# Kernel tuning notes

Measured on AMD Instinct MI355X. Metric: run time of the kernel, lower is better.

The kernel has to match this reference:

```python
import jax, jax.numpy as jnp
import numpy as np
import math

C = 91                      # num classes incl. background
BBOX_CLIP = math.log(1000.0 / 16.0)
IMG_H, IMG_W = 800.0, 800.0
SCORE_THRESH = 0.05
NMS_THRESH = 0.5
DETS_PER_IMG = 100
MIN_SIZE = 0.01
WX, WY, WW, WH = 10.0, 10.0, 5.0, 5.0   # bbox_reg_weights


def setup_inputs() -> dict:
    key = jax.random.key(0)
    ks = jax.random.split(key, 8)
    B, N, F_IN, HID = 4, 2048, 12544, 1024
    box_features = jax.random.normal(ks[0], (B, N, F_IN), jnp.float32) * 0.1
    # valid proposal boxes inside an 800x800 image: x1y1 in [0,600], wh in [10,200]
    xy = jax.random.uniform(ks[1], (B, N, 2), jnp.float32, minval=0.0, maxval=600.0)
    wh = jax.random.uniform(ks[2], (B, N, 2), jnp.float32, minval=10.0, maxval=200.0)
    proposals = jnp.concatenate([xy, xy + wh], axis=-1)
    def sc(k, sh, fan):
        return jax.random.normal(k, sh, jnp.float32) * (1.0 / np.sqrt(fan))
    return {
        'box_features': box_features,
        'proposals': proposals,
        'fc6_w': sc(ks[3], (F_IN, HID), F_IN), 'fc6_b': jnp.zeros((HID,), jnp.float32),
        'fc7_w': sc(ks[4], (HID, HID), HID),   'fc7_b': jnp.zeros((HID,), jnp.float32),
        'cls_w': sc(ks[5], (HID, C), HID),     'cls_b': jnp.zeros((C,), jnp.float32),
        'bbox_w': sc(ks[6], (HID, 4 * C), HID), 'bbox_b': jnp.zeros((4 * C,), jnp.float32),
    }


def decode_boxes(rel, props):
    w = props[:, 2] - props[:, 0]
    h = props[:, 3] - props[:, 1]
    cx = props[:, 0] + 0.5 * w
    cy = props[:, 1] + 0.5 * h
    dx = rel[..., 0] / WX
    dy = rel[..., 1] / WY
    dw = jnp.minimum(rel[..., 2] / WW, BBOX_CLIP)
    dh = jnp.minimum(rel[..., 3] / WH, BBOX_CLIP)
    pcx = dx * w[:, None] + cx[:, None]
    pcy = dy * h[:, None] + cy[:, None]
    pw = jnp.exp(dw) * w[:, None]
    ph = jnp.exp(dh) * h[:, None]
    return jnp.stack([pcx - 0.5 * pw, pcy - 0.5 * ph,
                      pcx + 0.5 * pw, pcy + 0.5 * ph], axis=-1)


def postprocess_one(logits, regr, props):
    # logits [N,C], regr [N,4C], props [N,4] -> padded top-DETS_PER_IMG detections
    N = logits.shape[0]
    boxes = decode_boxes(regr.reshape(N, C, 4), props)        # [N,C,4]
    scores = jax.nn.softmax(logits, axis=-1)                  # [N,C]
    # clip_boxes_to_image
    x = jnp.clip(boxes[..., 0::2], 0.0, IMG_W)
    y = jnp.clip(boxes[..., 1::2], 0.0, IMG_H)
    boxes = jnp.stack([x[..., 0], y[..., 0], x[..., 1], y[..., 1]], axis=-1)
    # drop background class, flatten candidates
    boxes = boxes[:, 1:].reshape(-1, 4)                       # [M,4], M=N*(C-1)
    scores = scores[:, 1:].reshape(-1)                        # [M]
    labels = jnp.broadcast_to(jnp.arange(1, C, dtype=jnp.int32)[None, :],
                              (N, C - 1)).reshape(-1)         # [M]
    # score threshold + remove_small_boxes (invalidate instead of dynamic gather)
    bw = boxes[:, 2] - boxes[:, 0]
    bh = boxes[:, 3] - boxes[:, 1]
    valid = (scores > SCORE_THRESH) & (bw >= MIN_SIZE) & (bh >= MIN_SIZE)
    s0 = jnp.where(valid, scores, -jnp.inf)
    # batched_nms via per-class coordinate offset
    offset = labels.astype(boxes.dtype)[:, None] * (max(IMG_H, IMG_W) + 1.0)
    ob = boxes + offset
    area = (ob[:, 2] - ob[:, 0]) * (ob[:, 3] - ob[:, 1])

    def body(sc_cur, _):
        best = jnp.argmax(sc_cur)
        bb = ob[best]
        lt = jnp.maximum(ob[:, :2], bb[:2])
        rb = jnp.minimum(ob[:, 2:], bb[2:])
        inter = jnp.prod(jnp.maximum(rb - lt, 0.0), axis=-1)
        union = jnp.maximum(area + area[best] - inter, 1e-6)
        iou = inter / union
        sc_new = jnp.where(iou > NMS_THRESH, -jnp.inf, sc_cur)
        return sc_new, (best, sc_cur[best])

    _, (keep, kept_s) = jax.lax.scan(body, s0, None, length=DETS_PER_IMG)
    ok = jnp.isfinite(kept_s)
    out_boxes = jnp.where(ok[:, None], boxes[keep], 0.0)      # [D,4]
    out_scores = jnp.where(ok, kept_s, 0.0)                   # [D]
    out_labels = jnp.where(ok, labels[keep], 0)               # [D] int32
    return out_boxes, out_scores, out_labels


def reference(box_features, proposals, fc6_w, fc6_b, fc7_w, fc7_b,
              cls_w, cls_b, bbox_w, bbox_b):
    # TwoMLPHead
    h = jax.nn.relu(box_features @ fc6_w + fc6_b)             # [B,N,1024]
    h = jax.nn.relu(h @ fc7_w + fc7_b)
    # FastRCNNPredictor
    logits = h @ cls_w + cls_b                                # [B,N,C]
    regr = h @ bbox_w + bbox_b                                # [B,N,4C]
    boxes, scores, labels = jax.vmap(postprocess_one)(logits, regr, proposals)
    return boxes, scores, labels
```

## Files before the change

### kernel.cpp

```cpp
#include <hip/hip_runtime.h>
#include <math.h>

#define NIMG   4
#define NPROP  2048
#define MTOT   8192
#define FIN    12544
#define HID    1024
#define NC     91
#define NCB    512
#define DETS   100
#define CAPMAX (NPROP * (NC - 1))
#define VLDS   2560

typedef __attribute__((ext_vector_type(8))) short short8;
typedef __attribute__((ext_vector_type(4))) float f32x4;

__device__ __forceinline__ unsigned short f2bf(float f) {
  union { float f; unsigned u; } v; v.f = f;
  unsigned r = v.u + 0x7fffu + ((v.u >> 16) & 1u);
  return (unsigned short)(r >> 16);
}

__device__ __forceinline__ unsigned cvtpk(float lo, float hi) {
  unsigned r;
  asm("v_cvt_pk_bf16_f32 %0, %1, %2" : "=v"(r) : "v"(lo), "v"(hi));
  return r;
}

__device__ __forceinline__ void gload_lds16(const void* g, void* l) {
  __builtin_amdgcn_global_load_lds((__attribute__((address_space(1))) void*)(g),
                                   (__attribute__((address_space(3))) void*)(l), 16, 0, 0);
}

__global__ void transpose_cvt(const float* __restrict__ in, unsigned short* __restrict__ out,
                              int K, int N, int row_off, int out_ld) {
  __shared__ float tile[32][33];
  int k0 = blockIdx.y * 32, n0 = blockIdx.x * 32;
  int tx = threadIdx.x, ty = threadIdx.y;
#pragma unroll
  for (int i = 0; i < 4; ++i) {
    int r = ty + i * 8;
    if (k0 + r < K && n0 + tx < N)
      tile[r][tx] = in[(size_t)(k0 + r) * N + (n0 + tx)];
  }
  __syncthreads();
#pragma unroll
  for (int i = 0; i < 4; ++i) {
    int r = ty + i * 8;
    if (n0 + r < N && k0 + tx < K)
      out[(size_t)(row_off + n0 + r) * out_ld + (k0 + tx)] = f2bf(tile[tx][r]);
  }
}

__global__ void prep_misc(unsigned short* __restrict__ Wcbt, float* __restrict__ bias_cb,
                          const float* __restrict__ cls_b, const float* __restrict__ bbox_b,
                          int* __restrict__ ccount) {
  int i = blockIdx.x * blockDim.x + threadIdx.x;
  int stride = gridDim.x * blockDim.x;
  for (int j = i; j < 57 * 1024; j += stride) Wcbt[455 * 1024 + j] = 0;
  for (int j = i; j < NCB; j += stride)
    bias_cb[j] = (j < 91) ? cls_b[j] : ((j < 455) ? bbox_b[j - 91] : 0.0f);
  if (i < NIMG) ccount[i] = 0;
}

template <bool AFP32, bool RELU, bool OUTBF16>
__global__ __launch_bounds__(256) void gemm_nt(const void* __restrict__ Av,
                                               const unsigned short* __restrict__ Bt,
                                               const float* __restrict__ bias,
                                               void* __restrict__ Cv,
                                               int M, int N, int K) {
  __shared__ __align__(16) unsigned short As[128 * 64];
  __shared__ __align__(16) unsigned short Bs[128 * 64];
  const int tid  = threadIdx.x;
  const int lane = tid & 63;
  const int wid  = tid >> 6;
  const int wm   = (wid >> 1) * 64;
  const int wn   = (wid & 1) * 64;
  const int m0   = blockIdx.y * 128, n0 = blockIdx.x * 128;
  const int lcol = lane & 15;
  const int lk8  = (lane >> 4) * 8;

  f32x4 acc[4][4];
#pragma unroll
  for (int a = 0; a < 4; ++a)
#pragma unroll
    for (int b = 0; b < 4; ++b)
#pragma unroll
      for (int r = 0; r < 4; ++r) acc[a][b][r] = 0.0f;

  const int st_r  = lane >> 3;
  const int st_kc = (lane & 7) << 3;

  for (int k0 = 0; k0 < K; k0 += 64) {
#pragma unroll
    for (int i = 0; i < 4; ++i) {
      int chunk = (wid << 2) | i;
      int r = (chunk << 3) | st_r;
      gload_lds16(Bt + (size_t)(n0 + r) * K + k0 + st_kc, Bs + (chunk << 9));
    }
    if constexpr (AFP32) {
#pragma unroll
      for (int i = 0; i < 4; ++i) {
        int s   = tid + (i << 8);
        int row = s >> 3;
        int kc  = (s & 7) << 3;
        const float* gp = (const float*)Av + (size_t)(m0 + row) * K + (k0 + kc);
        float4 u = *(const float4*)gp;
        float4 w = *(const float4*)(gp + 4);
        union { unsigned u32[4]; short8 s8; } pk;
        pk.u32[0] = cvtpk(u.x, u.y);
        pk.u32[1] = cvtpk(u.z, u.w);
        pk.u32[2] = cvtpk(w.x, w.y);
        pk.u32[3] = cvtpk(w.z, w.w);
        *(short8*)&As[row * 64 + kc] = pk.s8;
      }
    } else {
#pragma unroll
      for (int i = 0; i < 4; ++i) {
        int chunk = (wid << 2) | i;
        int r = (chunk << 3) | st_r;
        gload_lds16((const unsigned short*)Av + (size_t)(m0 + r) * K + k0 + st_kc,
                    As + (chunk << 9));
      }
    }
    __syncthreads();
#pragma unroll
    for (int kk = 0; kk < 64; kk += 32) {
      short8 af[4], bf[4];
#pragma unroll
      for (int im = 0; im < 4; ++im)
        af[im] = *(const short8*)&As[(wm + im * 16 + lcol) * 64 + kk + lk8];
#pragma unroll
      for (int in = 0; in < 4; ++in)
        bf[in] = *(const short8*)&Bs[(wn + in * 16 + lcol) * 64 + kk + lk8];
#pragma unroll
      for (int im = 0; im < 4; ++im)
#pragma unroll
        for (int in = 0; in < 4; ++in)
          acc[im][in] = __builtin_amdgcn_mfma_f32_16x16x32_bf16(af[im], bf[in], acc[im][in], 0, 0, 0);
    }
    __syncthreads();
  }

  const int r0 = (lane >> 4) * 4;
#pragma unroll
  for (int im = 0; im < 4; ++im) {
#pragma unroll
    for (int in = 0; in < 4; ++in) {
      int gn = n0 + wn + in * 16 + lcol;
      float bv = bias[gn];
#pragma unroll
      for (int r = 0; r < 4; ++r) {
        int gm = m0 + wm + im * 16 + r0 + r;
        float vv = acc[im][in][r] + bv;
        if (RELU) vv = fmaxf(vv, 0.0f);
        if (OUTBF16) ((unsigned short*)Cv)[(size_t)gm * N + gn] = f2bf(vv);
        else         ((float*)Cv)[(size_t)gm * N + gn] = vv;
      }
    }
  }
}

__global__ void candgen(const float* __restrict__ out3, const float* __restrict__ props,
                        float* __restrict__ cscore, float* __restrict__ cbox,
                        int* __restrict__ clabel, int* __restrict__ ccount, int CAP) {
  int gw   = (blockIdx.x * blockDim.x + threadIdx.x) >> 6;
  int lane = threadIdx.x & 63;
  if (gw >= MTOT) return;
  int img = gw >> 11;
  const float* row = out3 + (size_t)gw * NCB;

  float l0 = row[lane];
  float l1 = (lane < NC - 64) ? row[64 + lane] : -INFINITY;
  float mx = fmaxf(l0, l1);
#pragma unroll
  for (int off = 32; off; off >>= 1) mx = fmaxf(mx, __shfl_xor(mx, off));
  float e0 = expf(l0 - mx);
  float e1 = (lane < NC - 64) ? expf(l1 - mx) : 0.0f;
  float den = e0 + e1;
#pragma unroll
  for (int off = 32; off; off >>= 1) den += __shfl_xor(den, off);
  float inv = 1.0f / den;

  float4 p = *(const float4*)(props + (size_t)gw * 4);
  float w = p.z - p.x, h = p.w - p.y;
  float cx = p.x + 0.5f * w, cy = p.y + 0.5f * h;

#pragma unroll
  for (int half = 0; half < 2; ++half) {
    int c = (half << 6) + lane;
    float s = (half ? e1 : e0) * inv;
    if (c >= 1 && c < NC && s > 0.05f) {
      float dx = row[91 + c * 4 + 0] * 0.1f;
      float dy = row[91 + c * 4 + 1] * 0.1f;
      float dw = fminf(row[91 + c * 4 + 2] * 0.2f, 4.135166556742356f);
      float dh = fminf(row[91 + c * 4 + 3] * 0.2f, 4.135166556742356f);
      float pcx = dx * w + cx, pcy = dy * h + cy;
      float pw = expf(dw) * w, ph = expf(dh) * h;
      float x1 = fminf(fmaxf(pcx - 0.5f * pw, 0.0f), 800.0f);
      float x2 = fminf(fmaxf(pcx + 0.5f * pw, 0.0f), 800.0f);
      float y1 = fminf(fmaxf(pcy - 0.5f * ph, 0.0f), 800.0f);
      float y2 = fminf(fmaxf(pcy + 0.5f * ph, 0.0f), 800.0f);
      if (x2 - x1 >= 0.01f && y2 - y1 >= 0.01f) {
        int idx = atomicAdd(&ccount[img], 1);
        if (idx < CAP) {
          size_t o = (size_t)img * CAP + idx;
          cscore[o] = s;
          clabel[o] = c;
          cbox[o * 4 + 0] = x1; cbox[o * 4 + 1] = y1;
          cbox[o * 4 + 2] = x2; cbox[o * 4 + 3] = y2;
        }
      }
    }
  }
}

__global__ __launch_bounds__(256) void nms_kernel(float* __restrict__ cscore, const float* __restrict__ cbox,
                           const int* __restrict__ clabel, const int* __restrict__ ccount,
                           float* __restrict__ out, int CAP) {
  int img = blockIdx.x;
  int tid = threadIdx.x;
  int lane = tid & 63, wid = tid >> 6;
  int V = ccount[img]; if (V > CAP) V = CAP;
  int VL = V < VLDS ? V : VLDS;
  float* sc = cscore + (size_t)img * CAP;
  const float* bx = cbox + (size_t)img * CAP * 4;
  const int* lb = clabel + (size_t)img * CAP;
  float* ob  = out + (size_t)img * DETS * 4;
  float* osd = out + (size_t)NIMG * DETS * 4 + (size_t)img * DETS;
  float* ol  = out + (size_t)NIMG * DETS * 5 + (size_t)img * DETS;

  for (int t = tid; t < DETS; t += blockDim.x) {
    ob[t * 4 + 0] = 0.0f; ob[t * 4 + 1] = 0.0f; ob[t * 4 + 2] = 0.0f; ob[t * 4 + 3] = 0.0f;
    osd[t] = 0.0f; ol[t] = 0.0f;
  }

  __shared__ float sx1[VLDS], sy1[VLDS], sx2[VLDS], sy2[VLDS], sar[VLDS], ssc[VLDS];
  __shared__ float rs[4]; __shared__ int ri[4];
  __shared__ float bbs[6];
  __shared__ int   bbest;

  for (int t = tid; t < VL; t += blockDim.x) {
    float4 b = *(const float4*)&bx[(size_t)t * 4];
    float offv = (float)lb[t] * 801.0f;
    sx1[t] = b.x + offv; sy1[t] = b.y + offv;
    sx2[t] = b.z + offv; sy2[t] = b.w + offv;
    sar[t] = (b.z - b.x) * (b.w - b.y);
    ssc[t] = sc[t];
  }
  __syncthreads();

  for (int d = 0; d < DETS; ++d) {
    float bs = -INFINITY; int bi = -1;
    for (int t = tid; t < VL; t += blockDim.x) { float v = ssc[t]; if (v > bs) { bs = v; bi = t; } }
    if (V > VLDS)
      for (int t = VLDS + tid; t < V; t += blockDim.x) { float v = sc[t]; if (v > bs) { bs = v; bi = t; } }
#pragma unroll
    for (int off = 32; off; off >>= 1) {
      float osf = __shfl_xor(bs, off); int oi = __shfl_xor(bi, off);
      if (osf > bs) { bs = osf; bi = oi; }
    }
    if (lane == 0) { rs[wid] = bs; ri[wid] = bi; }
    __syncthreads();
    if (tid == 0) {
      float b0 = rs[0]; int i0 = ri[0];
      for (int wv = 1; wv < 4; ++wv) if (rs[wv] > b0) { b0 = rs[wv]; i0 = ri[wv]; }
      if (i0 < 0 || !(b0 > -INFINITY)) {
        bbest = -1;
      } else {
        bbest = i0;
        float ox1, oy1, ox2, oy2, ar;
        if (i0 < VLDS) { ox1 = sx1[i0]; oy1 = sy1[i0]; ox2 = sx2[i0]; oy2 = sy2[i0]; ar = sar[i0]; }
        else {
          float4 b = *(const float4*)&bx[(size_t)i0 * 4];
          float offv = (float)lb[i0] * 801.0f;
          ox1 = b.x + offv; oy1 = b.y + offv; ox2 = b.z + offv; oy2 = b.w + offv;
          ar = (b.z - b.x) * (b.w - b.y);
        }
        bbs[0] = ox1; bbs[1] = oy1; bbs[2] = ox2; bbs[3] = oy2; bbs[4] = ar;
        float4 rb = *(const float4*)&bx[(size_t)i0 * 4];
        ob[d * 4 + 0] = rb.x; ob[d * 4 + 1] = rb.y; ob[d * 4 + 2] = rb.z; ob[d * 4 + 3] = rb.w;
        osd[d] = b0;
        ol[d] = (float)lb[i0];
      }
    }
    __syncthreads();
    if (bbest < 0) break;
    float bx1 = bbs[0], by1 = bbs[1], bx2 = bbs[2], by2 = bbs[3], barea = bbs[4];
    for (int t = tid; t < VL; t += blockDim.x) {
      float ltx = fmaxf(sx1[t], bx1), lty = fmaxf(sy1[t], by1);
      float rbx = fminf(sx2[t], bx2), rby = fminf(sy2[t], by2);
      float inter = fmaxf(rbx - ltx, 0.0f) * fmaxf(rby - lty, 0.0f);
      float uni = fmaxf(sar[t] + barea - inter, 1e-6f);
      if (inter / uni > 0.5f) ssc[t] = -INFINITY;
    }
    if (V > VLDS) {
      for (int t = VLDS + tid; t < V; t += blockDim.x) {
        float4 b = *(const float4*)&bx[(size_t)t * 4];
        float offv = (float)lb[t] * 801.0f;
        float tx1 = b.x + offv, ty1 = b.y + offv, tx2 = b.z + offv, ty2 = b.w + offv;
        float ltx = fmaxf(tx1, bx1), lty = fmaxf(ty1, by1);
        float rbx = fminf(tx2, bx2), rby = fminf(ty2, by2);
        float inter = fmaxf(rbx - ltx, 0.0f) * fmaxf(rby - lty, 0.0f);
        float areat = (tx2 - tx1) * (ty2 - ty1);
        float uni = fmaxf(areat + barea - inter, 1e-6f);
        if (inter / uni > 0.5f) sc[t] = -INFINITY;
      }
    }
    __syncthreads();
  }
}

extern "C" void kernel_launch(void* const* d_in, const int* in_sizes, int n_in,
                              void* d_out, int out_size, void* d_ws, size_t ws_size,
                              hipStream_t stream) {
  const float* box_features = (const float*)d_in[0];
  const float* proposals    = (const float*)d_in[1];
  const float* fc6_w = (const float*)d_in[2];
  const float* fc6_b = (const float*)d_in[3];
  const float* fc7_w = (const float*)d_in[4];
  const float* fc7_b = (const float*)d_in[5];
  const float* cls_w = (const float*)d_in[6];
  const float* cls_b = (const float*)d_in[7];
  const float* bbox_w = (const float*)d_in[8];
  const float* bbox_b = (const float*)d_in[9];

  char* ws = (char*)d_ws;
  size_t off = 0;
  unsigned short* W6t  = (unsigned short*)(ws + off); off += (size_t)HID * FIN * 2;
  unsigned short* W7t  = (unsigned short*)(ws + off); off += (size_t)HID * HID * 2;
  unsigned short* Wcbt = (unsigned short*)(ws + off); off += (size_t)NCB * HID * 2;
  float* bias_cb       = (float*)(ws + off);          off += (size_t)NCB * 4;
  int*   ccount        = (int*)(ws + off);            off += 256;
  unsigned short* h1   = (unsigned short*)(ws + off); off += (size_t)MTOT * HID * 2;
  unsigned short* h2   = (unsigned short*)(ws + off); off += (size_t)MTOT * HID * 2;
  float* out3          = (float*)(ws + off);          off += (size_t)MTOT * NCB * 4;

  int CAP = CAPMAX;
  if (ws_size > off) {
    size_t avail = ws_size - off;
    size_t cap_ws = avail / 96;
    if (cap_ws < (size_t)CAP) CAP = (int)cap_ws;
  } else {
    CAP = 0;
  }
  float* cscore = (float*)(ws + off);
  int*   clabel = (int*)(ws + off + (size_t)NIMG * CAP * 4);
  float* cbox   = (float*)(ws + off + (size_t)NIMG * CAP * 8);

  transpose_cvt<<<dim3(HID / 32, FIN / 32), dim3(32, 8), 0, stream>>>(fc6_w, W6t, FIN, HID, 0, FIN);
  transpose_cvt<<<dim3(HID / 32, HID / 32), dim3(32, 8), 0, stream>>>(fc7_w, W7t, HID, HID, 0, HID);
  transpose_cvt<<<dim3(3,  HID / 32), dim3(32, 8), 0, stream>>>(cls_w,  Wcbt, HID, 91,  0,  HID);
  transpose_cvt<<<dim3(12, HID / 32), dim3(32, 8), 0, stream>>>(bbox_w, Wcbt, HID, 364, 91, HID);
  prep_misc<<<64, 256, 0, stream>>>(Wcbt, bias_cb, cls_b, bbox_b, ccount);

  gemm_nt<true,  true,  true ><<<dim3(HID / 128, MTOT / 128), 256, 0, stream>>>(
      box_features, W6t, fc6_b, h1, MTOT, HID, FIN);
  gemm_nt<false, true,  true ><<<dim3(HID / 128, MTOT / 128), 256, 0, stream>>>(
      h1, W7t, fc7_b, h2, MTOT, HID, HID);
  gemm_nt<false, false, false><<<dim3(NCB / 128, MTOT / 128), 256, 0, stream>>>(
      h2, Wcbt, bias_cb, out3, MTOT, NCB, HID);

  candgen<<<(MTOT * 64) / 256, 256, 0, stream>>>(out3, proposals, cscore, cbox, clabel, ccount, CAP);
  nms_kernel<<<NIMG, 256, 0, stream>>>(cscore, cbox, clabel, ccount, (float*)d_out, CAP);
}
```

Before: 1.011 ms.

## Double-buffer GEMM LDS tiles with XOR swizzle and swap grid mapping

The bf16 MFMA GEMM now uses two LDS buffers per operand, so the next K-tile's global loads (async LDS loads for B and bf16 A, register prefetch for fp32 A) are issued before computing the current tile. Only one barrier remains per iteration. LDS columns are XOR-swizzled by row to avoid bank conflicts on the short8 fragment reads. The grid is transposed so consecutive blocks walk M with a fixed N tile, which changes L2 reuse of the weight tiles. LDS use doubles to 64KB per block and the extra register prefetch may lower occupancy.

```diff
diff --git a/kernel.cpp b/kernel.cpp
--- a/kernel.cpp
+++ b/kernel.cpp
@@ -69,16 +69,20 @@
                                                const float* __restrict__ bias,
                                                void* __restrict__ Cv,
                                                int M, int N, int K) {
-  __shared__ __align__(16) unsigned short As[128 * 64];
-  __shared__ __align__(16) unsigned short Bs[128 * 64];
+  __shared__ __align__(16) unsigned short As[2][128 * 64];
+  __shared__ __align__(16) unsigned short Bs[2][128 * 64];
   const int tid  = threadIdx.x;
   const int lane = tid & 63;
   const int wid  = tid >> 6;
   const int wm   = (wid >> 1) * 64;
   const int wn   = (wid & 1) * 64;
-  const int m0   = blockIdx.y * 128, n0 = blockIdx.x * 128;
+  const int m0   = blockIdx.x * 128, n0 = blockIdx.y * 128;
   const int lcol = lane & 15;
-  const int lk8  = (lane >> 4) * 8;
+  const int lk4  = lane >> 4;
+  const int rsw  = lcol & 7;
+
+  const int st_r  = lane >> 3;
+  const int st_kc = ((lane & 7) ^ st_r) << 3;
 
   f32x4 acc[4][4];
 #pragma unroll
@@ -88,58 +92,77 @@
 #pragma unroll
       for (int r = 0; r < 4; ++r) acc[a][b][r] = 0.0f;
 
-  const int st_r  = lane >> 3;
-  const int st_kc = (lane & 7) << 3;
-
-  for (int k0 = 0; k0 < K; k0 += 64) {
+  const int NT = K >> 6;
+  float4 pa[4][2];
+
+  auto stage_async = [&](int buf, int t) {
+    const int k0 = t << 6;
 #pragma unroll
     for (int i = 0; i < 4; ++i) {
       int chunk = (wid << 2) | i;
       int r = (chunk << 3) | st_r;
-      gload_lds16(Bt + (size_t)(n0 + r) * K + k0 + st_kc, Bs + (chunk << 9));
-    }
-    if constexpr (AFP32) {
-#pragma unroll
-      for (int i = 0; i < 4; ++i) {
-        int s   = tid + (i << 8);
-        int row = s >> 3;
-        int kc  = (s & 7) << 3;
-        const float* gp = (const float*)Av + (size_t)(m0 + row) * K + (k0 + kc);
-        float4 u = *(const float4*)gp;
-        float4 w = *(const float4*)(gp + 4);
-        union { unsigned u32[4]; short8 s8; } pk;
-        pk.u32[0] = cvtpk(u.x, u.y);
-        pk.u32[1] = cvtpk(u.z, u.w);
-        pk.u32[2] = cvtpk(w.x, w.y);
-        pk.u32[3] = cvtpk(w.z, w.w);
-        *(short8*)&As[row * 64 + kc] = pk.s8;
-      }
-    } else {
-#pragma unroll
-      for (int i = 0; i < 4; ++i) {
-        int chunk = (wid << 2) | i;
-        int r = (chunk << 3) | st_r;
+      gload_lds16(Bt + (size_t)(n0 + r) * K + k0 + st_kc, &Bs[buf][chunk << 9]);
+      if constexpr (!AFP32)
         gload_lds16((const unsigned short*)Av + (size_t)(m0 + r) * K + k0 + st_kc,
-                    As + (chunk << 9));
-      }
-    }
-    __syncthreads();
-#pragma unroll
-    for (int kk = 0; kk < 64; kk += 32) {
+                    &As[buf][chunk << 9]);
+    }
+  };
+  auto loadA = [&](int t) {
+    const int k0 = t << 6;
+#pragma unroll
+    for (int i = 0; i < 4; ++i) {
+      int s = tid + (i << 8);
+      int row = s >> 3, kc = (s & 7) << 3;
+      const float* gp = (const float*)Av + (size_t)(m0 + row) * K + (k0 + kc);
+      pa[i][0] = *(const float4*)gp;
+      pa[i][1] = *(const float4*)(gp + 4);
+    }
+  };
+  auto writeA = [&](int buf) {
+#pragma unroll
+    for (int i = 0; i < 4; ++i) {
+      int s = tid + (i << 8);
+      int row = s >> 3;
+      int slot = ((s & 7) ^ (row & 7)) << 3;
+      union { unsigned u32[4]; short8 s8; } pk;
+      pk.u32[0] = cvtpk(pa[i][0].x, pa[i][0].y);
+      pk.u32[1] = cvtpk(pa[i][0].z, pa[i][0].w);
+      pk.u32[2] = cvtpk(pa[i][1].x, pa[i][1].y);
+      pk.u32[3] = cvtpk(pa[i][1].z, pa[i][1].w);
+      *(short8*)&As[buf][row * 64 + slot] = pk.s8;
+    }
+  };
+
+  stage_async(0, 0);
+  if constexpr (AFP32) { loadA(0); writeA(0); }
+  __syncthreads();
+
+  int cur = 0;
+  for (int t = 0; t < NT; ++t) {
+    const int nxt = cur ^ 1;
+    if (t + 1 < NT) {
+      stage_async(nxt, t + 1);
+      if constexpr (AFP32) loadA(t + 1);
+    }
+#pragma unroll
+    for (int kk = 0; kk < 2; ++kk) {
+      const int sb = kk << 2;
       short8 af[4], bf[4];
 #pragma unroll
       for (int im = 0; im < 4; ++im)
-        af[im] = *(const short8*)&As[(wm + im * 16 + lcol) * 64 + kk + lk8];
+        af[im] = *(const short8*)&As[cur][(wm + im * 16 + lcol) * 64 + (((sb + lk4) ^ rsw) << 3)];
 #pragma unroll
       for (int in = 0; in < 4; ++in)
-        bf[in] = *(const short8*)&Bs[(wn + in * 16 + lcol) * 64 + kk + lk8];
+        bf[in] = *(const short8*)&Bs[cur][(wn + in * 16 + lcol) * 64 + (((sb + lk4) ^ rsw) << 3)];
 #pragma unroll
       for (int im = 0; im < 4; ++im)
 #pragma unroll
         for (int in = 0; in < 4; ++in)
           acc[im][in] = __builtin_amdgcn_mfma_f32_16x16x32_bf16(af[im], bf[in], acc[im][in], 0, 0, 0);
     }
+    if (t + 1 < NT) { if constexpr (AFP32) writeA(nxt); }
     __syncthreads();
+    cur = nxt;
   }
 
   const int r0 = (lane >> 4) * 4;
@@ -354,11 +377,11 @@
   transpose_cvt<<<dim3(12, HID / 32), dim3(32, 8), 0, stream>>>(bbox_w, Wcbt, HID, 364, 91, HID);
   prep_misc<<<64, 256, 0, stream>>>(Wcbt, bias_cb, cls_b, bbox_b, ccount);
 
-  gemm_nt<true,  true,  true ><<<dim3(HID / 128, MTOT / 128), 256, 0, stream>>>(
+  gemm_nt<true,  true,  true ><<<dim3(MTOT / 128, HID / 128), 256, 0, stream>>>(
       box_features, W6t, fc6_b, h1, MTOT, HID, FIN);
-  gemm_nt<false, true,  true ><<<dim3(HID / 128, MTOT / 128), 256, 0, stream>>>(
+  gemm_nt<false, true,  true ><<<dim3(MTOT / 128, HID / 128), 256, 0, stream>>>(
       h1, W7t, fc7_b, h2, MTOT, HID, HID);
-  gemm_nt<false, false, false><<<dim3(NCB / 128, MTOT / 128), 256, 0, stream>>>(
+  gemm_nt<false, false, false><<<dim3(MTOT / 128, NCB / 128), 256, 0, stream>>>(
       h2, Wcbt, bias_cb, out3, MTOT, NCB, HID);
 
   candgen<<<(MTOT * 64) / 256, 256, 0, stream>>>(out3, proposals, cscore, cbox, clabel, ccount, CAP);
```

New measurement: 879.1 us. 1.15x faster.
